# Kernel optimization log

Hardware: AMD Instinct MI355X
Metric: run time of the kernel (lower is better)

The kernel has to match this reference:

```python
import jax, jax.numpy as jnp
import numpy as np

N_LAYERS = 2
DIN = 128
DOUT = 128


def _uniform(key, shape, std):
    return jax.random.uniform(key, shape, jnp.float32, -std, std)


def setup_inputs() -> dict:
    key = jax.random.key(0)
    ks = jax.random.split(key, 12)
    B, T, N, F = 2, 8, 10000, DIN
    E = 320000
    x = jax.random.normal(ks[0], (B, T, N, F), jnp.float32)
    edge_index = jax.random.randint(ks[1], (2, E), 0, N, jnp.int64)
    edge_weight = jax.random.uniform(ks[2], (E,), jnp.float32)
    std_w = 1.0 / np.sqrt(DOUT)
    std_p = 1.0 / np.sqrt(DIN)
    std_g = 1.0 / np.sqrt(DIN)  # torch GRUCell init: U(-1/sqrt(H), 1/sqrt(H))
    W0 = _uniform(ks[3], (N_LAYERS, DIN, DOUT), std_w)
    p = _uniform(ks[4], (N_LAYERS, DIN, 1), std_p)
    w_ih = _uniform(ks[5], (N_LAYERS, 3 * DIN, DIN), std_g)
    w_hh = _uniform(ks[6], (N_LAYERS, 3 * DIN, DIN), std_g)
    b_ih = _uniform(ks[7], (N_LAYERS, 3 * DIN), std_g)
    b_hh = _uniform(ks[8], (N_LAYERS, 3 * DIN), std_g)
    bias = jnp.zeros((N_LAYERS, DOUT), jnp.float32)
    return {"x": x, "edge_index": edge_index, "edge_weight": edge_weight,
            "W0": W0, "p": p, "w_ih": w_ih, "w_hh": w_hh,
            "b_ih": b_ih, "b_hh": b_hh, "bias": bias}


def _gru_cell(xg, hg, wih, whh, bih, bhh):
    # torch.nn.GRUCell: gate order r, z, n
    gi = xg @ wih.T + bih
    gh = hg @ whh.T + bhh
    ir, iz, inn = jnp.split(gi, 3, axis=-1)
    hr, hz, hn = jnp.split(gh, 3, axis=-1)
    r = jax.nn.sigmoid(ir + hr)
    z = jax.nn.sigmoid(iz + hz)
    n = jnp.tanh(inn + r * hn)
    return (1.0 - z) * n + z * hg


def _topk_pool(xb, pc, k):
    # xb: [b, N, din], pc: [din, 1] -> [b, k, din]
    scores = (xb @ pc)[..., 0] / jnp.linalg.norm(pc)  # [b, N]
    vals, idx = jax.lax.top_k(scores, k)               # [b, k], sorted desc
    g = jnp.take_along_axis(xb, idx[..., None], axis=1)  # [b, k, din]
    return g * jnp.tanh(vals)[..., None]


def reference(x, edge_index, edge_weight, W0, p, w_ih, w_hh, b_ih, b_hh, bias):
    B, T, N, F = x.shape
    dout = W0.shape[-1]
    # --- GCN symmetric normalization with self-loops (done once, static graph) ---
    src, tgt = edge_index[0], edge_index[1]
    loops = jnp.arange(N, dtype=src.dtype)
    row = jnp.concatenate([src, loops])
    col = jnp.concatenate([tgt, loops])
    w = jnp.concatenate([edge_weight, jnp.ones((N,), x.dtype)])
    deg = jnp.zeros((N,), x.dtype).at[col].add(w)
    dinv = jnp.where(deg > 0, deg ** -0.5, 0.0)
    wn = dinv[row] * w * dinv[col]  # [E+N]

    def step(Ws, xt):
        out = xt  # [b, N, din]
        new_Ws = []
        for c in range(N_LAYERS):
            W = Ws[c]  # [b, din, dout]
            din = W.shape[1]
            pooled = _topk_pool(out, p[c], dout)                 # [b, dout, din]
            hg = W.transpose(0, 2, 1).reshape(B * dout, din)     # (b dout) din
            xg = pooled.reshape(B * dout, din)
            hg = _gru_cell(xg, hg, w_ih[c], w_hh[c], b_ih[c], b_hh[c])
            W = hg.reshape(B, dout, din).transpose(0, 2, 1)      # [b, din, dout]
            o = jnp.einsum('bnd,bde->bne', out, W)               # [b, N, dout]
            # gather-scale-scatter propagation (aggr='add')
            m = o[:, row, :] * wn[None, :, None]                 # [b, E+N, dout]
            o = jnp.zeros((B, N, dout), x.dtype).at[:, col, :].add(m)
            o = o + bias[c]
            out = jax.nn.relu(o)
            new_Ws.append(W)
        return tuple(new_Ws), out

    Ws0 = tuple(jnp.broadcast_to(W0[c], (B,) + W0[c].shape) for c in range(N_LAYERS))
    _, outs = jax.lax.scan(step, Ws0, jnp.moveaxis(x, 1, 0))
    return outs[-1]  # output at final step, [b, N, hidden]
```

## Files before the change

### kernel.cpp

```cpp
#include <hip/hip_runtime.h>
#include <hip/hip_bf16.h>
#include <math.h>


#define BB 2
#define TT 8
#define FF 128
#define GG 384
#define BINS 8192
#define CAP 512

__device__ __forceinline__ float bf2f(unsigned short u) {
  return __uint_as_float((unsigned)u << 16);
}
__device__ __forceinline__ unsigned short f2bf(float f) {
  unsigned x = __float_as_uint(f);
  unsigned r = ((x >> 16) & 1u) + 0x7fffu;
  return (unsigned short)((x + r) >> 16);
}

__global__ void prep_kernel(const int* __restrict__ ei32, int E, int* __restrict__ flag,
                            const float* __restrict__ p, float* __restrict__ pinv) {
  if (blockIdx.x == 0) {
    int step = E / 256;
    int e = threadIdx.x * step;
    if (ei32[2 * e + 1] != 0) *flag = 1;
  } else {
    int c = blockIdx.x - 1, tid = threadIdx.x;
    float s = 0.f;
    if (tid < 128) { float v = p[c * FF + tid]; s = v * v; }
    for (int o = 32; o; o >>= 1) s += __shfl_xor(s, o, 64);
    __shared__ float red[4];
    if ((tid & 63) == 0) red[tid >> 6] = s;
    __syncthreads();
    if (tid == 0) pinv[c] = 1.0f / sqrtf(red[0] + red[1] + red[2] + red[3]);
  }
}

__device__ __forceinline__ void edge_fetch(const void* ei, int is32, int E,
                                           int e, const float* ew,
                                           int& row, int& col, float& w) {
  if (e < E) {
    if (is32) {
      const int* p = (const int*)ei;
      row = p[e]; col = p[E + e];
    } else {
      const long long* p = (const long long*)ei;
      row = (int)p[e]; col = (int)p[(long long)E + e];
    }
    w = ew[e];
  } else {
    row = col = e - E; w = 1.0f;
  }
}

__global__ void hist_kernel(const void* ei, const int* flag, int E, int N,
                            const float* __restrict__ ew,
                            float* __restrict__ deg, int* __restrict__ counts) {
  int e = blockIdx.x * 256 + threadIdx.x;
  if (e >= E + N) return;
  int row, col; float w;
  edge_fetch(ei, *flag, E, e, ew, row, col, w);
  atomicAdd(&deg[col], w);
  atomicAdd(&counts[col], 1);
}

__global__ __launch_bounds__(1024) void scan_kernel(
    const int* __restrict__ counts, const float* __restrict__ deg,
    int* __restrict__ offsets, float* __restrict__ dinv, int N, int EN) {
  __shared__ int wtot[16];
  int tid = threadIdx.x, lane = tid & 63, wid = tid >> 6;
  int base = tid * 10;
  int lc[10]; int s10 = 0;
#pragma unroll
  for (int q = 0; q < 10; ++q) {
    int idx = base + q;
    int cv = (idx < N) ? counts[idx] : 0;
    lc[q] = cv; s10 += cv;
    if (idx < N) {
      float d = deg[idx];
      dinv[idx] = (d > 0.f) ? 1.0f / sqrtf(d) : 0.f;
    }
  }
  int s = s10;
#pragma unroll
  for (int off = 1; off <= 32; off <<= 1) {
    int v = __shfl_up(s, off, 64);
    if (lane >= off) s += v;
  }
  if (lane == 63) wtot[wid] = s;
  __syncthreads();
  int pre = 0;
  for (int w2 = 0; w2 < wid; ++w2) pre += wtot[w2];
  int run = pre + s - s10;
#pragma unroll
  for (int q = 0; q < 10; ++q) {
    int idx = base + q;
    if (idx < N) { offsets[idx] = run; run += lc[q]; }
  }
  if (tid == 0) offsets[N] = EN;
}

__global__ void scatter_kernel(const void* ei, const int* flag, int E, int N,
                               const float* __restrict__ ew,
                               const float* __restrict__ dinv,
                               const int* __restrict__ offs,
                               int* __restrict__ cursors,
                               int2* __restrict__ ep) {
  int e = blockIdx.x * 256 + threadIdx.x;
  if (e >= E + N) return;
  int row, col; float w;
  edge_fetch(ei, *flag, E, e, ew, row, col, w);
  int pos = atomicAdd(&cursors[col], 1);
  ep[offs[col] + pos] = make_int2(row, __float_as_int(dinv[row] * w * dinv[col]));
}

template <int SRC_BF16>
__global__ __launch_bounds__(256) void prop_kernel(
    const void* __restrict__ srcv, size_t s_tstride, size_t s_bstride,
    float* __restrict__ dst, size_t d_tstride, size_t d_bstride,
    const int2* __restrict__ ep, const int* __restrict__ offs,
    const float* __restrict__ p, const float* __restrict__ pinv,
    unsigned long long* __restrict__ keys, int* __restrict__ hist, int N) {
  int t = blockIdx.y;
  int lane = threadIdx.x & 63;
  int v = blockIdx.x * 4 + (threadIdx.x >> 6);
  if (v >= N) return;
  int e0 = offs[v], e1 = offs[v + 1];
  size_t o0 = ((size_t)t * s_tstride) >> 1, o1 = o0 + (s_bstride >> 1);
  const float2* f0 = (const float2*)srcv + o0;
  const float2* f1 = (const float2*)srcv + o1;
  const ushort2* u0 = (const ushort2*)srcv + o0;
  const ushort2* u1 = (const ushort2*)srcv + o1;
  float2 acc0 = {0.f, 0.f}, acc1 = {0.f, 0.f};
  for (int base = e0; base < e1; base += 64) {
    int cnt = e1 - base; if (cnt > 64) cnt = 64;
    int2 m = make_int2(0, 0);
    if (lane < cnt) m = ep[base + lane];
    for (int i = 0; i < cnt; ++i) {
      int si = __shfl(m.x, i, 64);
      float wv = __int_as_float(__shfl(m.y, i, 64));
      size_t r = (size_t)si * 64 + lane;
      float2 x0, x1;
      if constexpr (SRC_BF16) {
        ushort2 a = u0[r], b = u1[r];
        x0 = make_float2(bf2f(a.x), bf2f(a.y));
        x1 = make_float2(bf2f(b.x), bf2f(b.y));
      } else {
        x0 = f0[r]; x1 = f1[r];
      }
      acc0.x += wv * x0.x; acc0.y += wv * x0.y;
      acc1.x += wv * x1.x; acc1.y += wv * x1.y;
    }
  }
  float2* d0 = (float2*)(dst + (size_t)t * d_tstride);
  float2* d1 = (float2*)(dst + (size_t)t * d_tstride + d_bstride);
  d0[(size_t)v * 64 + lane] = acc0;
  d1[(size_t)v * 64 + lane] = acc1;
  if constexpr (!SRC_BF16) {
    if (p) {
      float2 pp = ((const float2*)p)[lane];
      float2 xv0 = f0[(size_t)v * 64 + lane], xv1 = f1[(size_t)v * 64 + lane];
      float sc0 = xv0.x * pp.x + xv0.y * pp.y;
      float sc1 = xv1.x * pp.x + xv1.y * pp.y;
      for (int o = 32; o; o >>= 1) {
        sc0 += __shfl_xor(sc0, o, 64);
        sc1 += __shfl_xor(sc1, o, 64);
      }
      if (lane == 0) {
        float piv = *pinv;
        float ss[2] = {sc0 * piv, sc1 * piv};
#pragma unroll
        for (int b = 0; b < 2; ++b) {
          unsigned u = __float_as_uint(ss[b]);
          u = (u & 0x80000000u) ? ~u : (u | 0x80000000u);
          int tb = t * 2 + b;
          keys[(size_t)tb * N + v] =
              ((unsigned long long)u << 32) | (unsigned)(~v);
          atomicAdd(&hist[tb * BINS + (u >> 19)], 1);
        }
      }
    }
  }
}

__device__ __forceinline__ unsigned long long shfl_xor_u64(unsigned long long x,
                                                           int m) {
  unsigned lo = (unsigned)x, hi = (unsigned)(x >> 32);
  lo = __shfl_xor(lo, m, 64);
  hi = __shfl_xor(hi, m, 64);
  return ((unsigned long long)hi << 32) | lo;
}

__global__ __launch_bounds__(1024) void selectsort_kernel(
    const unsigned long long* __restrict__ keys, const int* __restrict__ hist,
    int N, int* __restrict__ idx_sel, float* __restrict__ gate_sel) {
  int tb = blockIdx.y * 2 + blockIdx.x, tid = threadIdx.x;
  int lane = tid & 63, wid = tid >> 6;
  const int* h = hist + tb * BINS;
  __shared__ int wtot[16];
  __shared__ unsigned long long cand[CAP];
  __shared__ int sT, ncnt;
  int base = tid * 8;
  int lc[8]; int local = 0;
#pragma unroll
  for (int q = 0; q < 8; ++q) { lc[q] = h[base + q]; local += lc[q]; }
  if (tid == 0) ncnt = 0;
  int s = local;
#pragma unroll
  for (int off = 1; off <= 32; off <<= 1) {
    int v = __shfl_down(s, off, 64);
    if (lane + off < 64) s += v;
  }
  if (lane == 0) wtot[wid] = s;
  __syncthreads();
  int above_w = 0;
  for (int w2 = wid + 1; w2 < 16; ++w2) above_w += wtot[w2];
  int incl = above_w + s;
  int above = incl - local;
  if (above < 128 && incl >= 128) {
    int cnt = above;
#pragma unroll
    for (int q = 7; q >= 0; --q) {
      int c = lc[q];
      if (cnt + c >= 128) { sT = base + q; break; }
      cnt += c;
    }
  }
  __syncthreads();
  int T = sT;
  for (int i = tid; i < N; i += 1024) {
    unsigned long long kk = keys[(size_t)tb * N + i];
    if ((int)(kk >> 51) >= T) {
      int pos = atomicAdd(&ncnt, 1);
      if (pos < CAP) cand[pos] = kk;
    }
  }
  __syncthreads();
  if (tid < 64) {
    int nc = ncnt < CAP ? ncnt : CAP;
    unsigned long long v[8];
#pragma unroll
    for (int r = 0; r < 8; ++r) {
      int e = r * 64 + lane;
      v[r] = (e < nc) ? cand[e] : 0ULL;
    }
    for (int k = 2; k <= 512; k <<= 1)
      for (int j = k >> 1; j > 0; j >>= 1) {
        if (j >= 64) {
          int rj = j >> 6;
#pragma unroll
          for (int r = 0; r < 8; ++r)
            if (!(r & rj)) {
              int r2 = r | rj;
              bool up = (((r * 64) & k) != 0);
              unsigned long long a = v[r], c = v[r2];
              bool sw = up ? (a > c) : (a < c);
              if (sw) { v[r] = c; v[r2] = a; }
            }
        } else {
#pragma unroll
          for (int r = 0; r < 8; ++r) {
            unsigned long long o = shfl_xor_u64(v[r], j);
            int e = r * 64 + lane;
            bool up = (e & k) != 0;
            bool lower = (lane & j) == 0;
            unsigned long long mn = v[r] < o ? v[r] : o;
            unsigned long long mx = v[r] < o ? o : v[r];
            v[r] = (lower == up) ? mn : mx;
          }
        }
      }
#pragma unroll
    for (int r = 0; r < 2; ++r) {
      int e = r * 64 + lane;
      unsigned long long kk = v[r];
      unsigned n = ~((unsigned)kk);
      unsigned u = (unsigned)(kk >> 32);
      float sc = (u & 0x80000000u) ? __uint_as_float(u & 0x7FFFFFFFu)
                                   : __uint_as_float(~u);
      idx_sel[tb * 128 + e] = (int)n;
      gate_sel[tb * 128 + e] = tanhf(sc);
    }
  }
}

template <int SRC_BF16>
__global__ __launch_bounds__(256) void wchain_kernel(
    const void* __restrict__ srcv, size_t src_tstride, size_t src_bstride,
    const int* __restrict__ idx_sel, const float* __restrict__ gate_sel,
    const float* __restrict__ Winit,
    const float* __restrict__ wih, const float* __restrict__ whh,
    const float* __restrict__ bih, const float* __restrict__ bhh,
    float* __restrict__ snap) {
  int b = blockIdx.x, j0 = blockIdx.y * 8;
  int tid = threadIdx.x, side = tid >> 7, kl = tid & 127;
  __shared__ float pooled[8][FF];
  __shared__ float hbuf[8][FF];
  __shared__ float ghbuf[3][8][FF];
  for (int e = tid; e < 8 * FF; e += 256) {
    int j = e >> 7, m = e & 127;
    hbuf[j][m] = Winit[m * FF + j0 + j];
  }
  float b0 = side ? bhh[kl] : bih[kl];
  float b1 = side ? bhh[FF + kl] : bih[FF + kl];
  float b2 = side ? bhh[2 * FF + kl] : bih[2 * FF + kl];
  const float* wmat = side ? whh : wih;
  const float4* w0p = (const float4*)(wmat + (size_t)(0 * FF + kl) * FF);
  const float4* w1p = (const float4*)(wmat + (size_t)(1 * FF + kl) * FF);
  const float4* w2p = (const float4*)(wmat + (size_t)(2 * FF + kl) * FF);
  for (int t = 0; t < TT; ++t) {
    int tb = t * 2 + b;
    __syncthreads();
    for (int e = tid; e < 8 * FF; e += 256) {
      int j = e >> 7, m = e & 127;
      int n = idx_sel[tb * 128 + j0 + j];
      float g = gate_sel[tb * 128 + j0 + j];
      size_t off = (size_t)t * src_tstride + (size_t)b * src_bstride +
                   (size_t)n * FF + m;
      float xv;
      if constexpr (SRC_BF16) xv = bf2f(((const unsigned short*)srcv)[off]);
      else                    xv = ((const float*)srcv)[off];
      pooled[j][m] = xv * g;
    }
    __syncthreads();
    const float4* vsrc = (const float4*)(side ? &hbuf[0][0] : &pooled[0][0]);
    float acc0[8] = {}, acc1[8] = {}, acc2[8] = {};
    for (int mq = 0; mq < 32; ++mq) {
      float4 w0 = w0p[mq], w1 = w1p[mq], w2 = w2p[mq];
#pragma unroll
      for (int j = 0; j < 8; ++j) {
        float4 v = vsrc[j * 32 + mq];
        acc0[j] += v.x * w0.x + v.y * w0.y + v.z * w0.z + v.w * w0.w;
        acc1[j] += v.x * w1.x + v.y * w1.y + v.z * w1.z + v.w * w1.w;
        acc2[j] += v.x * w2.x + v.y * w2.y + v.z * w2.z + v.w * w2.w;
      }
    }
    if (side) {
#pragma unroll
      for (int j = 0; j < 8; ++j) {
        ghbuf[0][j][kl] = acc0[j] + b0;
        ghbuf[1][j][kl] = acc1[j] + b1;
        ghbuf[2][j][kl] = acc2[j] + b2;
      }
    }
    __syncthreads();
    if (!side) {
#pragma unroll
      for (int j = 0; j < 8; ++j) {
        float rr = 1.0f / (1.0f + expf(-(acc0[j] + b0 + ghbuf[0][j][kl])));
        float zz = 1.0f / (1.0f + expf(-(acc1[j] + b1 + ghbuf[1][j][kl])));
        float nn = tanhf(acc2[j] + b2 + rr * ghbuf[2][j][kl]);
        float h = hbuf[j][kl];
        float hn = (1.0f - zz) * nn + zz * h;
        hbuf[j][kl] = hn;
        snap[((size_t)tb * FF + kl) * FF + j0 + j] = hn;
      }
    }
  }
}

__global__ __launch_bounds__(256) void gemm_kernel(
    const float* __restrict__ A, size_t a_tstride, size_t a_bstride,
    const float* __restrict__ Wsnap, const float* __restrict__ bias,
    float* __restrict__ outf, unsigned short* __restrict__ outb,
    size_t o_tstride, size_t o_bstride,
    const float* __restrict__ p1, const float* __restrict__ pinv1,
    unsigned long long* __restrict__ keys, int* __restrict__ hist, int N) {
  int nb = blockIdx.x, b = blockIdx.y, t = blockIdx.z;
  int tb = t * 2 + b;
  __shared__ float Ast[32][132];
  __shared__ float Bs[32][128];
  __shared__ float spart[128][17];
  __shared__ float p1s[128];
  int tid = threadIdx.x;
  int tc = tid & 15, tr = tid >> 4;
  if (p1 && tid < 128) p1s[tid] = p1[tid];
  float acc[8][8] = {};
  const float* Ab = A + (size_t)t * a_tstride + (size_t)b * a_bstride;
  const float* Wb = Wsnap + (size_t)tb * FF * FF;
  for (int kc = 0; kc < 4; ++kc) {
    int k0 = kc * 32;
    __syncthreads();
    for (int e = tid; e < 128 * 32; e += 256) {
      int r = e >> 5, kk = e & 31;
      int n = nb * 128 + r;
      Ast[kk][r] = (n < N) ? Ab[(size_t)n * FF + k0 + kk] : 0.f;
    }
    for (int e = tid; e < 32 * 128; e += 256) {
      int r = e >> 7, dd = e & 127;
      Bs[r][dd] = Wb[(k0 + r) * FF + dd];
    }
    __syncthreads();
#pragma unroll 4
    for (int kk = 0; kk < 32; ++kk) {
      const float4* arow = (const float4*)Ast[kk];
      float4 a0 = arow[tr * 2], a1 = arow[tr * 2 + 1];
      const float4* brow = (const float4*)Bs[kk];
      float4 b0 = brow[tc * 2], b1 = brow[tc * 2 + 1];
      float av[8] = {a0.x, a0.y, a0.z, a0.w, a1.x, a1.y, a1.z, a1.w};
      float bv[8] = {b0.x, b0.y, b0.z, b0.w, b1.x, b1.y, b1.z, b1.w};
#pragma unroll
      for (int i = 0; i < 8; ++i)
#pragma unroll
        for (int j = 0; j < 8; ++j) acc[i][j] += av[i] * bv[j];
    }
  }
  float bb[8];
#pragma unroll
  for (int j = 0; j < 8; ++j) bb[j] = bias[tc * 8 + j];
  size_t obase = (size_t)t * o_tstride + (size_t)b * o_bstride;
#pragma unroll
  for (int i = 0; i < 8; ++i) {
    int n = nb * 128 + tr * 8 + i;
    float v[8]; float part = 0.f;
#pragma unroll
    for (int j = 0; j < 8; ++j) {
      v[j] = fmaxf(acc[i][j] + bb[j], 0.f);
      if (p1) part += v[j] * p1s[tc * 8 + j];
    }
    if (n < N) {
      if (outb) {
        unsigned short* dst = outb + obase + (size_t)n * FF + tc * 8;
        uint4 pk;
        pk.x = (unsigned)f2bf(v[0]) | ((unsigned)f2bf(v[1]) << 16);
        pk.y = (unsigned)f2bf(v[2]) | ((unsigned)f2bf(v[3]) << 16);
        pk.z = (unsigned)f2bf(v[4]) | ((unsigned)f2bf(v[5]) << 16);
        pk.w = (unsigned)f2bf(v[6]) | ((unsigned)f2bf(v[7]) << 16);
        *(uint4*)dst = pk;
      } else {
        float4* dst = (float4*)(outf + obase + (size_t)n * FF + tc * 8);
        dst[0] = make_float4(v[0], v[1], v[2], v[3]);
        dst[1] = make_float4(v[4], v[5], v[6], v[7]);
      }
    }
    if (p1) spart[tr * 8 + i][tc] = part;
  }
  if (p1) {
    __syncthreads();
    if (tid < 128) {
      int n = nb * 128 + tid;
      if (n < N) {
        float s = 0.f;
#pragma unroll
        for (int q = 0; q < 16; ++q) s += spart[tid][q];
        s *= *pinv1;
        unsigned u = __float_as_uint(s);
        u = (u & 0x80000000u) ? ~u : (u | 0x80000000u);
        keys[(size_t)tb * N + n] = ((unsigned long long)u << 32) | (unsigned)(~n);
        atomicAdd(&hist[tb * BINS + (u >> 19)], 1);
      }
    }
  }
}

extern "C" void kernel_launch(void* const* d_in, const int* in_sizes, int n_in,
                              void* d_out, int out_size, void* d_ws, size_t ws_size,
                              hipStream_t stream) {
  const float* x   = (const float*)d_in[0];
  const void*  ei  = d_in[1];
  const float* ew  = (const float*)d_in[2];
  const float* W0  = (const float*)d_in[3];
  const float* p   = (const float*)d_in[4];
  const float* wih = (const float*)d_in[5];
  const float* whh = (const float*)d_in[6];
  const float* bih = (const float*)d_in[7];
  const float* bhh = (const float*)d_in[8];
  const float* bias= (const float*)d_in[9];

  const int E  = in_sizes[2];
  const int N  = in_sizes[0] / (BB * TT * FF);
  const int EN = E + N;
  const size_t NF = (size_t)N * FF;

  char* w = (char*)d_ws;
  auto alloc = [&](size_t bytes) -> char* {
    char* r = w; w += (bytes + 255) & ~(size_t)255; return r;
  };
  char* zbeg = w;
  float* deg      = (float*)alloc((size_t)N * 4);
  int*   counts   = (int*)  alloc((size_t)N * 4);
  int*   cursors  = (int*)  alloc((size_t)N * 4);
  int*   flag     = (int*)  alloc(4);
  int*   hist     = (int*)  alloc((size_t)2 * TT * BB * BINS * 4);
  char* zend = w;
  int*   offsets  = (int*)  alloc((size_t)(N + 1) * 4);
  float* dinv     = (float*)alloc((size_t)N * 4);
  float* pinv     = (float*)alloc(2 * 4);
  int2*  ep       = (int2*) alloc((size_t)EN * 8);
  unsigned long long* keys0 = (unsigned long long*)alloc((size_t)TT * BB * N * 8);
  unsigned long long* keys1 = (unsigned long long*)alloc((size_t)TT * BB * N * 8);
  int*   idx0     = (int*)  alloc((size_t)TT * BB * 128 * 4);
  float* gate0    = (float*)alloc((size_t)TT * BB * 128 * 4);
  int*   idx1     = (int*)  alloc((size_t)TT * BB * 128 * 4);
  float* gate1    = (float*)alloc((size_t)TT * BB * 128 * 4);
  float* W0snap   = (float*)alloc((size_t)TT * BB * FF * FF * 4);
  float* W1snap   = (float*)alloc((size_t)TT * BB * FF * FF * 4);
  float* xp       = (float*)alloc((size_t)TT * BB * NF * 4);
  unsigned short* act0 = (unsigned short*)alloc((size_t)TT * BB * NF * 2);
  float* xq       = (float*)alloc((size_t)BB * NF * 4);
  int* hist0 = hist;
  int* hist1 = hist + (size_t)TT * BB * BINS;

  hipMemsetAsync(zbeg, 0, (size_t)(zend - zbeg), stream);

  prep_kernel<<<3, 256, 0, stream>>>((const int*)ei, E, flag, p, pinv);
  hist_kernel<<<(EN + 255) / 256, 256, 0, stream>>>(ei, flag, E, N, ew, deg, counts);
  scan_kernel<<<1, 1024, 0, stream>>>(counts, deg, offsets, dinv, N, EN);
  scatter_kernel<<<(EN + 255) / 256, 256, 0, stream>>>(ei, flag, E, N, ew, dinv,
                                                       offsets, cursors, ep);

  prop_kernel<0><<<dim3((N + 3) / 4, TT), 256, 0, stream>>>(
      x, NF, (size_t)TT * NF, xp, (size_t)BB * NF, NF,
      ep, offsets, p, pinv, keys0, hist0, N);

  selectsort_kernel<<<dim3(BB, TT), 1024, 0, stream>>>(
      keys0, hist0, N, idx0, gate0);

  wchain_kernel<0><<<dim3(BB, 16), 256, 0, stream>>>(
      x, NF, (size_t)TT * NF, idx0, gate0, W0,
      wih, whh, bih, bhh, W0snap);

  gemm_kernel<<<dim3((N + 127) / 128, BB, TT), 256, 0, stream>>>(
      xp, (size_t)BB * NF, NF, W0snap, bias,
      nullptr, act0, (size_t)BB * NF, NF,
      p + FF, pinv + 1, keys1, hist1, N);

  selectsort_kernel<<<dim3(BB, TT), 1024, 0, stream>>>(
      keys1, hist1, N, idx1, gate1);

  wchain_kernel<1><<<dim3(BB, 16), 256, 0, stream>>>(
      act0, (size_t)BB * NF, NF, idx1, gate1, W0 + FF * FF,
      wih + (size_t)GG * FF, whh + (size_t)GG * FF,
      bih + GG, bhh + GG, W1snap);

  prop_kernel<1><<<dim3((N + 3) / 4, 1), 256, 0, stream>>>(
      act0 + (size_t)(TT - 1) * BB * NF, 0, NF, xq, 0, NF,
      ep, offsets, nullptr, nullptr, nullptr, nullptr, N);

  gemm_kernel<<<dim3((N + 127) / 128, BB, 1), 256, 0, stream>>>(
      xq, 0, NF, W1snap + (size_t)(TT - 1) * BB * FF * FF, bias + FF,
      (float*)d_out, nullptr, 0, NF,
      nullptr, nullptr, nullptr, nullptr, N);
}
```

Baseline: 972.1 us.

## Split propagation wave into half-waves gathering float4 rows, and double wchain grid

The propagation kernel now has each half of a 64-lane wave handle a different edge. Each lane loads 4 features (float4 or 4 bf16), so every iteration works on 4 edges with 2 independent gathers per lane. The two halves are combined with a cross-half shuffle before a nontemporal store. This aims to cut loop overhead per edge and raise memory-level parallelism in the gather-bound propagation. Separately, the GRU chain kernel handles 4 columns per block instead of 8 and launches twice as many blocks, giving more parallelism to the serial time-step chain at the cost of reloading the weights in more blocks.

```diff
diff --git a/kernel.cpp b/kernel.cpp
--- a/kernel.cpp
+++ b/kernel.cpp
@@ -10,6 +10,8 @@
 #define BINS 8192
 #define CAP 512
 
+typedef float v4f __attribute__((ext_vector_type(4)));
+
 __device__ __forceinline__ float bf2f(unsigned short u) {
   return __uint_as_float((unsigned)u << 16);
 }
@@ -17,6 +19,9 @@
   unsigned x = __float_as_uint(f);
   unsigned r = ((x >> 16) & 1u) + 0x7fffu;
   return (unsigned short)((x + r) >> 16);
+}
+__device__ __forceinline__ float4 bf4(ushort4 u) {
+  return make_float4(bf2f(u.x), bf2f(u.y), bf2f(u.z), bf2f(u.w));
 }
 
 __global__ void prep_kernel(const int* __restrict__ ei32, int E, int* __restrict__ flag,
@@ -124,61 +129,71 @@
     unsigned long long* __restrict__ keys, int* __restrict__ hist, int N) {
   int t = blockIdx.y;
   int lane = threadIdx.x & 63;
+  int half = lane >> 5, sub = lane & 31;
   int v = blockIdx.x * 4 + (threadIdx.x >> 6);
   if (v >= N) return;
   int e0 = offs[v], e1 = offs[v + 1];
-  size_t o0 = ((size_t)t * s_tstride) >> 1, o1 = o0 + (s_bstride >> 1);
-  const float2* f0 = (const float2*)srcv + o0;
-  const float2* f1 = (const float2*)srcv + o1;
-  const ushort2* u0 = (const ushort2*)srcv + o0;
-  const ushort2* u1 = (const ushort2*)srcv + o1;
-  float2 acc0 = {0.f, 0.f}, acc1 = {0.f, 0.f};
+  size_t o0 = (size_t)t * s_tstride, o1 = o0 + s_bstride;
+  const float4* f0 = (const float4*)srcv + (o0 >> 2);
+  const float4* f1 = (const float4*)srcv + (o1 >> 2);
+  const ushort4* u0 = (const ushort4*)srcv + (o0 >> 2);
+  const ushort4* u1 = (const ushort4*)srcv + (o1 >> 2);
+  float4 acc0 = {0.f, 0.f, 0.f, 0.f}, acc1 = {0.f, 0.f, 0.f, 0.f};
   for (int base = e0; base < e1; base += 64) {
     int cnt = e1 - base; if (cnt > 64) cnt = 64;
     int2 m = make_int2(0, 0);
     if (lane < cnt) m = ep[base + lane];
-    for (int i = 0; i < cnt; ++i) {
-      int si = __shfl(m.x, i, 64);
-      float wv = __int_as_float(__shfl(m.y, i, 64));
-      size_t r = (size_t)si * 64 + lane;
-      float2 x0, x1;
+    for (int i = 0; i < cnt; i += 4) {
+      int i0 = i + half, i1 = i + 2 + half;
+      int sA = __shfl(m.x, i0, 64);
+      float wA = __int_as_float(__shfl(m.y, i0, 64));
+      int sB = __shfl(m.x, i1, 64);
+      float wB = __int_as_float(__shfl(m.y, i1, 64));
+      if (i0 >= cnt) wA = 0.f;
+      if (i1 >= cnt) wB = 0.f;
+      size_t rA = (size_t)sA * 32 + sub, rB = (size_t)sB * 32 + sub;
+      float4 a0, a1, b0, b1;
       if constexpr (SRC_BF16) {
-        ushort2 a = u0[r], b = u1[r];
-        x0 = make_float2(bf2f(a.x), bf2f(a.y));
-        x1 = make_float2(bf2f(b.x), bf2f(b.y));
+        a0 = bf4(u0[rA]); a1 = bf4(u1[rA]);
+        b0 = bf4(u0[rB]); b1 = bf4(u1[rB]);
       } else {
-        x0 = f0[r]; x1 = f1[r];
-      }
-      acc0.x += wv * x0.x; acc0.y += wv * x0.y;
-      acc1.x += wv * x1.x; acc1.y += wv * x1.y;
-    }
-  }
-  float2* d0 = (float2*)(dst + (size_t)t * d_tstride);
-  float2* d1 = (float2*)(dst + (size_t)t * d_tstride + d_bstride);
-  d0[(size_t)v * 64 + lane] = acc0;
-  d1[(size_t)v * 64 + lane] = acc1;
+        a0 = f0[rA]; a1 = f1[rA];
+        b0 = f0[rB]; b1 = f1[rB];
+      }
+      acc0.x += wA * a0.x + wB * b0.x;  acc0.y += wA * a0.y + wB * b0.y;
+      acc0.z += wA * a0.z + wB * b0.z;  acc0.w += wA * a0.w + wB * b0.w;
+      acc1.x += wA * a1.x + wB * b1.x;  acc1.y += wA * a1.y + wB * b1.y;
+      acc1.z += wA * a1.z + wB * b1.z;  acc1.w += wA * a1.w + wB * b1.w;
+    }
+  }
+  acc0.x += __shfl_xor(acc0.x, 32, 64); acc0.y += __shfl_xor(acc0.y, 32, 64);
+  acc0.z += __shfl_xor(acc0.z, 32, 64); acc0.w += __shfl_xor(acc0.w, 32, 64);
+  acc1.x += __shfl_xor(acc1.x, 32, 64); acc1.y += __shfl_xor(acc1.y, 32, 64);
+  acc1.z += __shfl_xor(acc1.z, 32, 64); acc1.w += __shfl_xor(acc1.w, 32, 64);
+  if (half == 0) {
+    v4f* d0 = (v4f*)((float4*)(dst + (size_t)t * d_tstride) +
+                     (size_t)v * 32 + sub);
+    v4f* d1 = (v4f*)((float4*)(dst + (size_t)t * d_tstride + d_bstride) +
+                     (size_t)v * 32 + sub);
+    v4f s0 = {acc0.x, acc0.y, acc0.z, acc0.w};
+    v4f s1 = {acc1.x, acc1.y, acc1.z, acc1.w};
+    __builtin_nontemporal_store(s0, d0);
+    __builtin_nontemporal_store(s1, d1);
+  }
   if constexpr (!SRC_BF16) {
     if (p) {
-      float2 pp = ((const float2*)p)[lane];
-      float2 xv0 = f0[(size_t)v * 64 + lane], xv1 = f1[(size_t)v * 64 + lane];
-      float sc0 = xv0.x * pp.x + xv0.y * pp.y;
-      float sc1 = xv1.x * pp.x + xv1.y * pp.y;
-      for (int o = 32; o; o >>= 1) {
-        sc0 += __shfl_xor(sc0, o, 64);
-        sc1 += __shfl_xor(sc1, o, 64);
-      }
-      if (lane == 0) {
-        float piv = *pinv;
-        float ss[2] = {sc0 * piv, sc1 * piv};
-#pragma unroll
-        for (int b = 0; b < 2; ++b) {
-          unsigned u = __float_as_uint(ss[b]);
-          u = (u & 0x80000000u) ? ~u : (u | 0x80000000u);
-          int tb = t * 2 + b;
-          keys[(size_t)tb * N + v] =
-              ((unsigned long long)u << 32) | (unsigned)(~v);
-          atomicAdd(&hist[tb * BINS + (u >> 19)], 1);
-        }
+      float4 xv = (half ? f1 : f0)[(size_t)v * 32 + sub];
+      float4 pp = ((const float4*)p)[sub];
+      float sc = xv.x * pp.x + xv.y * pp.y + xv.z * pp.z + xv.w * pp.w;
+#pragma unroll
+      for (int o = 1; o <= 16; o <<= 1) sc += __shfl_xor(sc, o, 64);
+      if (sub == 0) {
+        float ss = sc * (*pinv);
+        unsigned u = __float_as_uint(ss);
+        u = (u & 0x80000000u) ? ~u : (u | 0x80000000u);
+        int tb = t * 2 + half;
+        keys[(size_t)tb * N + v] = ((unsigned long long)u << 32) | (unsigned)(~v);
+        atomicAdd(&hist[tb * BINS + (u >> 19)], 1);
       }
     }
   }
@@ -293,12 +308,12 @@
     const float* __restrict__ wih, const float* __restrict__ whh,
     const float* __restrict__ bih, const float* __restrict__ bhh,
     float* __restrict__ snap) {
-  int b = blockIdx.x, j0 = blockIdx.y * 8;
+  int b = blockIdx.x, j0 = blockIdx.y * 4;
   int tid = threadIdx.x, side = tid >> 7, kl = tid & 127;
-  __shared__ float pooled[8][FF];
-  __shared__ float hbuf[8][FF];
-  __shared__ float ghbuf[3][8][FF];
-  for (int e = tid; e < 8 * FF; e += 256) {
+  __shared__ float pooled[4][FF];
+  __shared__ float hbuf[4][FF];
+  __shared__ float ghbuf[3][4][FF];
+  for (int e = tid; e < 4 * FF; e += 256) {
     int j = e >> 7, m = e & 127;
     hbuf[j][m] = Winit[m * FF + j0 + j];
   }
@@ -312,7 +327,7 @@
   for (int t = 0; t < TT; ++t) {
     int tb = t * 2 + b;
     __syncthreads();
-    for (int e = tid; e < 8 * FF; e += 256) {
+    for (int e = tid; e < 4 * FF; e += 256) {
       int j = e >> 7, m = e & 127;
       int n = idx_sel[tb * 128 + j0 + j];
       float g = gate_sel[tb * 128 + j0 + j];
@@ -325,11 +340,11 @@
     }
     __syncthreads();
     const float4* vsrc = (const float4*)(side ? &hbuf[0][0] : &pooled[0][0]);
-    float acc0[8] = {}, acc1[8] = {}, acc2[8] = {};
+    float acc0[4] = {}, acc1[4] = {}, acc2[4] = {};
     for (int mq = 0; mq < 32; ++mq) {
       float4 w0 = w0p[mq], w1 = w1p[mq], w2 = w2p[mq];
 #pragma unroll
-      for (int j = 0; j < 8; ++j) {
+      for (int j = 0; j < 4; ++j) {
         float4 v = vsrc[j * 32 + mq];
         acc0[j] += v.x * w0.x + v.y * w0.y + v.z * w0.z + v.w * w0.w;
         acc1[j] += v.x * w1.x + v.y * w1.y + v.z * w1.z + v.w * w1.w;
@@ -338,7 +353,7 @@
     }
     if (side) {
 #pragma unroll
-      for (int j = 0; j < 8; ++j) {
+      for (int j = 0; j < 4; ++j) {
         ghbuf[0][j][kl] = acc0[j] + b0;
         ghbuf[1][j][kl] = acc1[j] + b1;
         ghbuf[2][j][kl] = acc2[j] + b2;
@@ -347,7 +362,7 @@
     __syncthreads();
     if (!side) {
 #pragma unroll
-      for (int j = 0; j < 8; ++j) {
+      for (int j = 0; j < 4; ++j) {
         float rr = 1.0f / (1.0f + expf(-(acc0[j] + b0 + ghbuf[0][j][kl])));
         float zz = 1.0f / (1.0f + expf(-(acc1[j] + b1 + ghbuf[1][j][kl])));
         float nn = tanhf(acc2[j] + b2 + rr * ghbuf[2][j][kl]);
@@ -517,7 +532,7 @@
   selectsort_kernel<<<dim3(BB, TT), 1024, 0, stream>>>(
       keys0, hist0, N, idx0, gate0);
 
-  wchain_kernel<0><<<dim3(BB, 16), 256, 0, stream>>>(
+  wchain_kernel<0><<<dim3(BB, 32), 256, 0, stream>>>(
       x, NF, (size_t)TT * NF, idx0, gate0, W0,
       wih, whh, bih, bhh, W0snap);
 
@@ -529,7 +544,7 @@
   selectsort_kernel<<<dim3(BB, TT), 1024, 0, stream>>>(
       keys1, hist1, N, idx1, gate1);
 
-  wchain_kernel<1><<<dim3(BB, 16), 256, 0, stream>>>(
+  wchain_kernel<1><<<dim3(BB, 32), 256, 0, stream>>>(
       act0, (size_t)BB * NF, NF, idx1, gate1, W0 + FF * FF,
       wih + (size_t)GG * FF, whh + (size_t)GG * FF,
       bih + GG, bhh + GG, W1snap);
```

Measured after the change: 919.3 us. -5.4%, faster.
